# Kernel tuning notes

Hardware: AMD Instinct MI355X
Metric: run time of the kernel (lower is better)

The kernel has to match this reference:

```python
import jax, jax.numpy as jnp
import numpy as np

BLOCK_M, BLOCK_K = 16, 64
THRES = 0.8


def setup_inputs() -> dict:
    key = jax.random.key(0)
    kx, kw = jax.random.split(key)
    bsz, seq, in_f, out_f = 128, 1, 4096, 11008
    x = jax.random.normal(kx, (bsz, seq, in_f), dtype=jnp.float16)
    # kaiming_uniform_(a=sqrt(5)) on a (in,out) weight -> bound = 1/sqrt(fan_in)
    bound = 1.0 / np.sqrt(in_f)
    weight = jax.random.uniform(kw, (in_f, out_f), dtype=jnp.float16,
                                minval=-bound, maxval=bound)
    bias = jnp.zeros((out_f,), dtype=jnp.float16)
    return {"x": x, "weight": weight, "bias": bias}


def reference(x, weight, bias):
    bsz, seq, hidden = x.shape
    x2 = x.reshape(bsz * seq, hidden)          # (M, K), seq == 1 decode path
    M, K = x2.shape
    # avg_magnitude_threshold: per (BLOCK_M, BLOCK_K) block mean |x| vs thres
    blocks = x2.reshape(M // BLOCK_M, BLOCK_M, K // BLOCK_K, BLOCK_K)
    avg = jnp.mean(jnp.abs(blocks).astype(jnp.float32), axis=(1, 3))  # (M/bm, K/bk)
    mask = avg > THRES                           # block active if avg magnitude above thres
    # blocksparse_masked_gemm: skipped blocks contribute nothing -> zero them out
    xm = jnp.where(mask[:, None, :, None], blocks, jnp.float16(0)).reshape(M, K)
    y = xm @ weight                              # (M, out_features)
    return y.reshape(bsz, seq, -1) + bias
```

## Files before the change

### kernel.cpp

```cpp
#include <hip/hip_runtime.h>
#include <stdint.h>

using f32x4   = __attribute__((ext_vector_type(4))) float;
using short8  = __attribute__((ext_vector_type(8))) short;
using float4v = __attribute__((ext_vector_type(4))) float;
using float2v = __attribute__((ext_vector_type(2))) float;
using uint2v  = __attribute__((ext_vector_type(2))) unsigned int;

#define NCOL 11008
#define KDIM 4096
#define LSTRIDE 264

__device__ __forceinline__ unsigned pk_bf16(float a, float b) {
  unsigned ua = __float_as_uint(a); ua += 0x7fffu + ((ua >> 16) & 1u);
  unsigned ub = __float_as_uint(b); ub += 0x7fffu + ((ub >> 16) & 1u);
  return (ua >> 16) | (ub & 0xffff0000u);
}

__global__ __launch_bounds__(256) void mask_kernel(const float* __restrict__ x,
                                                   unsigned* __restrict__ mask16) {
  const int rb  = blockIdx.x >> 2;
  const int grp = blockIdx.x & 3;
  const int t   = threadIdx.x;
  __shared__ double part[256];
  double s = 0.0;
#pragma unroll 4
  for (int i = 0; i < 16; ++i) {
    const float* p = x + (size_t)(rb * 16 + i) * KDIM + grp * 1024 + t * 4;
    float4v a = *(const float4v*)p;
    s += (double)fabsf(a[0]) + (double)fabsf(a[1]) +
         (double)fabsf(a[2]) + (double)fabsf(a[3]);
  }
  part[t] = s;
  __syncthreads();
  if (t < 16) {
    double acc = 0.0;
#pragma unroll
    for (int u = 0; u < 16; ++u) acc += part[t * 16 + u];
    bool on = (acc * (1.0 / 1024.0)) > (double)0.8f;
    unsigned long long bal = __ballot(on);
    if (t == 0) mask16[blockIdx.x] = (unsigned)(bal & 0xffffu);
  }
}

__global__ __launch_bounds__(256) void gemm_kernel(
    const float* __restrict__ x, const float* __restrict__ w,
    const float* __restrict__ bias, const unsigned* __restrict__ mask16,
    float* __restrict__ out) {

  __shared__ __align__(16) uint8_t lds[64 * LSTRIDE];

  const int tid  = threadIdx.x;
  const int lane = tid & 63;
  const int wv   = tid >> 6;
  const int c    = lane & 15;
  const int q    = lane >> 4;
  const int rb   = blockIdx.x;
  const int n0   = blockIdx.y * 128;

  unsigned long long bm = 0;
#pragma unroll
  for (int g = 0; g < 4; ++g)
    bm |= ((unsigned long long)mask16[rb * 4 + g]) << (16 * g);

  f32x4 acc[2] = {};

  const int sk = tid >> 5;
  const int sn = (tid & 31) * 4;
  uint8_t* wS = lds + (size_t)sk * LSTRIDE + sn * 2;

  for (int kb = 0; kb < 64; ++kb) {
    if (!((bm >> kb) & 1ull)) continue;

    const float* wp = w + (size_t)(kb * 64 + sk) * NCOL + n0 + sn;
    float4v wr[8];
#pragma unroll
    for (int r = 0; r < 8; ++r)
      wr[r] = *(const float4v*)(wp + (size_t)r * 8 * NCOL);

    __syncthreads();
#pragma unroll
    for (int r = 0; r < 8; ++r) {
      uint2v v;
      v[0] = pk_bf16(wr[r][0], wr[r][1]);
      v[1] = pk_bf16(wr[r][2], wr[r][3]);
      *(uint2v*)(wS + (size_t)r * 8 * LSTRIDE) = v;
    }
    __syncthreads();

#pragma unroll
    for (int ks = 0; ks < 2; ++ks) {
      const float* xp = x + (size_t)(rb * 16 + c) * KDIM + kb * 64 + ks * 32 + q * 8;
      float4v xa = *(const float4v*)xp;
      float4v xb = *(const float4v*)(xp + 4);
      union { short8 v; unsigned u[4]; } af;
      af.u[0] = pk_bf16(xa[0], xa[1]);
      af.u[1] = pk_bf16(xa[2], xa[3]);
      af.u[2] = pk_bf16(xb[0], xb[1]);
      af.u[3] = pk_bf16(xb[2], xb[3]);

      const uint8_t* wb = lds + (size_t)(ks * 32 + q * 8) * LSTRIDE + (wv * 32 + 2 * c) * 2;
      unsigned wj[8];
#pragma unroll
      for (int j = 0; j < 8; ++j)
        wj[j] = *(const unsigned*)(wb + (size_t)j * LSTRIDE);
      union { short8 v; unsigned u[4]; } be, bo;
#pragma unroll
      for (int p = 0; p < 4; ++p) {
        be.u[p] = (wj[2 * p] & 0x0000ffffu) | (wj[2 * p + 1] << 16);
        bo.u[p] = (wj[2 * p] >> 16) | (wj[2 * p + 1] & 0xffff0000u);
      }
      acc[0] = __builtin_amdgcn_mfma_f32_16x16x32_bf16(af.v, be.v, acc[0], 0, 0, 0);
      acc[1] = __builtin_amdgcn_mfma_f32_16x16x32_bf16(af.v, bo.v, acc[1], 0, 0, 0);
    }
  }

  const int colE = n0 + wv * 32 + 2 * c;
  const float bE = bias[colE];
  const float bO = bias[colE + 1];
#pragma unroll
  for (int p = 0; p < 4; ++p) {
    const int row = rb * 16 + q * 4 + p;
    float2v st;
    st[0] = acc[0][p] + bE;
    st[1] = acc[1][p] + bO;
    *(float2v*)(out + (size_t)row * NCOL + colE) = st;
  }
}

extern "C" void kernel_launch(void* const* d_in, const int* in_sizes, int n_in,
                              void* d_out, int out_size, void* d_ws, size_t ws_size,
                              hipStream_t stream) {
  const float* x    = (const float*)d_in[0];
  const float* w    = (const float*)d_in[1];
  const float* bias = (const float*)d_in[2];
  float* out        = (float*)d_out;
  unsigned* mask16  = (unsigned*)d_ws;

  hipLaunchKernelGGL(mask_kernel, dim3(32), dim3(256), 0, stream, x, mask16);
  hipLaunchKernelGGL(gemm_kernel, dim3(8, 86), dim3(256), 0, stream,
                     x, w, bias, mask16, out);
}
```

Measured before the change: 298.7 us.

## Prefetch next active block's weights and activations while computing current block

The GEMM loop now walks only the set bits of the block mask using ctz, and issues the global loads for the next active K-block right after the current block's weights are written to LDS, so those loads overlap the MFMA work. Activation loads are also hoisted into registers as part of this prefetch. The mask kernel's row loop is fully unrolled. The cost is higher register pressure from holding the prefetched weight and activation registers alongside the current block's data.

```diff
diff --git a/kernel.cpp b/kernel.cpp
--- a/kernel.cpp
+++ b/kernel.cpp
@@ -24,7 +24,7 @@
   const int t   = threadIdx.x;
   __shared__ double part[256];
   double s = 0.0;
-#pragma unroll 4
+#pragma unroll
   for (int i = 0; i < 16; ++i) {
     const float* p = x + (size_t)(rb * 16 + i) * KDIM + grp * 1024 + t * 4;
     float4v a = *(const float4v*)p;
@@ -68,15 +68,31 @@
   const int sk = tid >> 5;
   const int sn = (tid & 31) * 4;
   uint8_t* wS = lds + (size_t)sk * LSTRIDE + sn * 2;
+  const float* xrow = x + (size_t)(rb * 16 + c) * KDIM + q * 8;
 
-  for (int kb = 0; kb < 64; ++kb) {
-    if (!((bm >> kb) & 1ull)) continue;
+  float4v wr[8];
+  float4v xr[4];
 
-    const float* wp = w + (size_t)(kb * 64 + sk) * NCOL + n0 + sn;
-    float4v wr[8];
-#pragma unroll
-    for (int r = 0; r < 8; ++r)
-      wr[r] = *(const float4v*)(wp + (size_t)r * 8 * NCOL);
+#define ISSUE(KB)                                                        \
+  {                                                                      \
+    const float* wp = w + (size_t)((KB)*64 + sk) * NCOL + n0 + sn;       \
+    _Pragma("unroll")                                                    \
+    for (int r = 0; r < 8; ++r)                                          \
+      wr[r] = *(const float4v*)(wp + (size_t)r * 8 * NCOL);              \
+    const float* xp = xrow + (KB)*64;                                    \
+    xr[0] = *(const float4v*)(xp);                                       \
+    xr[1] = *(const float4v*)(xp + 4);                                   \
+    xr[2] = *(const float4v*)(xp + 32);                                  \
+    xr[3] = *(const float4v*)(xp + 36);                                  \
+  }
+
+  unsigned long long rem = bm;
+  int kb = -1;
+  if (rem) { kb = __builtin_ctzll(rem); rem &= rem - 1; ISSUE(kb); }
+
+  while (kb >= 0) {
+    int kbn = -1;
+    if (rem) { kbn = __builtin_ctzll(rem); rem &= rem - 1; }
 
     __syncthreads();
 #pragma unroll
@@ -88,16 +104,23 @@
     }
     __syncthreads();
 
+    float4v xs0 = xr[0], xs1 = xr[1], xs2 = xr[2], xs3 = xr[3];
+    if (kbn >= 0) ISSUE(kbn);
+
 #pragma unroll
     for (int ks = 0; ks < 2; ++ks) {
-      const float* xp = x + (size_t)(rb * 16 + c) * KDIM + kb * 64 + ks * 32 + q * 8;
-      float4v xa = *(const float4v*)xp;
-      float4v xb = *(const float4v*)(xp + 4);
       union { short8 v; unsigned u[4]; } af;
-      af.u[0] = pk_bf16(xa[0], xa[1]);
-      af.u[1] = pk_bf16(xa[2], xa[3]);
-      af.u[2] = pk_bf16(xb[0], xb[1]);
-      af.u[3] = pk_bf16(xb[2], xb[3]);
+      if (ks == 0) {
+        af.u[0] = pk_bf16(xs0[0], xs0[1]);
+        af.u[1] = pk_bf16(xs0[2], xs0[3]);
+        af.u[2] = pk_bf16(xs1[0], xs1[1]);
+        af.u[3] = pk_bf16(xs1[2], xs1[3]);
+      } else {
+        af.u[0] = pk_bf16(xs2[0], xs2[1]);
+        af.u[1] = pk_bf16(xs2[2], xs2[3]);
+        af.u[2] = pk_bf16(xs3[0], xs3[1]);
+        af.u[3] = pk_bf16(xs3[2], xs3[3]);
+      }
 
       const uint8_t* wb = lds + (size_t)(ks * 32 + q * 8) * LSTRIDE + (wv * 32 + 2 * c) * 2;
       unsigned wj[8];
@@ -113,7 +136,9 @@
       acc[0] = __builtin_amdgcn_mfma_f32_16x16x32_bf16(af.v, be.v, acc[0], 0, 0, 0);
       acc[1] = __builtin_amdgcn_mfma_f32_16x16x32_bf16(af.v, bo.v, acc[1], 0, 0, 0);
     }
+    kb = kbn;
   }
+#undef ISSUE
 
   const int colE = n0 + wv * 32 + 2 * c;
   const float bE = bias[colE];
```

Measured after the change: 303.1 us. About the same (+1.5%).

## Pre-convert masked activations to bf16 and split-K GEMM with full-M weight reuse

Applied to the files above, without the earlier changes.

A combined kernel now computes the block mask and writes zeroed-or-converted bf16 activations to the workspace. The GEMM no longer skips inactive K blocks per row block. Each workgroup covers all 128 rows for a 128-column tile and a 512-wide K slice, so each weight tile is loaded once instead of eight times, with a software prefetch of the next weight tile. Partial sums go to the output through float atomics after a memset, which adds a memset launch and atomic traffic and gives up per-row-block sparsity skipping.

```diff
diff --git a/kernel.cpp b/kernel.cpp
--- a/kernel.cpp
+++ b/kernel.cpp
@@ -6,6 +6,7 @@
 using float4v = __attribute__((ext_vector_type(4))) float;
 using float2v = __attribute__((ext_vector_type(2))) float;
 using uint2v  = __attribute__((ext_vector_type(2))) unsigned int;
+using uint4v  = __attribute__((ext_vector_type(4))) unsigned int;
 
 #define NCOL 11008
 #define KDIM 4096
@@ -17,36 +18,45 @@
   return (ua >> 16) | (ub & 0xffff0000u);
 }
 
-__global__ __launch_bounds__(256) void mask_kernel(const float* __restrict__ x,
-                                                   unsigned* __restrict__ mask16) {
-  const int rb  = blockIdx.x >> 2;
-  const int grp = blockIdx.x & 3;
-  const int t   = threadIdx.x;
+__global__ __launch_bounds__(256) void mask_convert_kernel(
+    const float* __restrict__ x, unsigned* __restrict__ xbf) {
+  const int rb = blockIdx.x;
+  const int g  = blockIdx.y;
+  const int t  = threadIdx.x;
   __shared__ double part[256];
+  __shared__ unsigned sh_bits;
+
+  const float* base = x + (size_t)rb * 16 * KDIM + g * 512 + t * 2;
   double s = 0.0;
-#pragma unroll 4
-  for (int i = 0; i < 16; ++i) {
-    const float* p = x + (size_t)(rb * 16 + i) * KDIM + grp * 1024 + t * 4;
-    float4v a = *(const float4v*)p;
-    s += (double)fabsf(a[0]) + (double)fabsf(a[1]) +
-         (double)fabsf(a[2]) + (double)fabsf(a[3]);
+#pragma unroll
+  for (int r = 0; r < 16; ++r) {
+    float2v a = *(const float2v*)(base + (size_t)r * KDIM);
+    s += (double)fabsf(a[0]) + (double)fabsf(a[1]);
   }
   part[t] = s;
   __syncthreads();
-  if (t < 16) {
+  if (t < 8) {
     double acc = 0.0;
 #pragma unroll
-    for (int u = 0; u < 16; ++u) acc += part[t * 16 + u];
+    for (int u = 0; u < 32; ++u) acc += part[t * 32 + u];
     bool on = (acc * (1.0 / 1024.0)) > (double)0.8f;
     unsigned long long bal = __ballot(on);
-    if (t == 0) mask16[blockIdx.x] = (unsigned)(bal & 0xffffu);
+    if (t == 0) sh_bits = (unsigned)(bal & 0xffu);
+  }
+  __syncthreads();
+  const unsigned keep = (sh_bits >> (t >> 5)) & 1u;
+
+  unsigned* dst = xbf + (size_t)rb * 16 * (KDIM / 2) + g * 256 + t;
+#pragma unroll
+  for (int r = 0; r < 16; ++r) {
+    float2v a = *(const float2v*)(base + (size_t)r * KDIM);
+    dst[(size_t)r * (KDIM / 2)] = keep ? pk_bf16(a[0], a[1]) : 0u;
   }
 }
 
 __global__ __launch_bounds__(256) void gemm_kernel(
-    const float* __restrict__ x, const float* __restrict__ w,
-    const float* __restrict__ bias, const unsigned* __restrict__ mask16,
-    float* __restrict__ out) {
+    const unsigned* __restrict__ xbf, const float* __restrict__ w,
+    const float* __restrict__ bias, float* __restrict__ out) {
 
   __shared__ __align__(16) uint8_t lds[64 * LSTRIDE];
 
@@ -55,29 +65,28 @@
   const int wv   = tid >> 6;
   const int c    = lane & 15;
   const int q    = lane >> 4;
-  const int rb   = blockIdx.x;
-  const int n0   = blockIdx.y * 128;
+  const int n0   = blockIdx.x * 128;
+  const int kz   = blockIdx.y;
 
-  unsigned long long bm = 0;
-#pragma unroll
-  for (int g = 0; g < 4; ++g)
-    bm |= ((unsigned long long)mask16[rb * 4 + g]) << (16 * g);
-
-  f32x4 acc[2] = {};
+  f32x4 acc[8][2] = {};
 
   const int sk = tid >> 5;
   const int sn = (tid & 31) * 4;
   uint8_t* wS = lds + (size_t)sk * LSTRIDE + sn * 2;
 
-  for (int kb = 0; kb < 64; ++kb) {
-    if (!((bm >> kb) & 1ull)) continue;
+  float4v wr[8];
+#define ISSUE_W(KB)                                                      \
+  {                                                                      \
+    const float* wp = w + (size_t)(kz * 512 + (KB)*64 + sk) * NCOL + n0 + sn; \
+    _Pragma("unroll")                                                    \
+    for (int r = 0; r < 8; ++r)                                          \
+      wr[r] = *(const float4v*)(wp + (size_t)r * 8 * NCOL);              \
+  }
 
-    const float* wp = w + (size_t)(kb * 64 + sk) * NCOL + n0 + sn;
-    float4v wr[8];
-#pragma unroll
-    for (int r = 0; r < 8; ++r)
-      wr[r] = *(const float4v*)(wp + (size_t)r * 8 * NCOL);
+  const uint4v* aBase = (const uint4v*)xbf + (size_t)c * 512 + kz * 64 + q;
 
+  ISSUE_W(0);
+  for (int kb = 0; kb < 8; ++kb) {
     __syncthreads();
 #pragma unroll
     for (int r = 0; r < 8; ++r) {
@@ -87,17 +96,14 @@
       *(uint2v*)(wS + (size_t)r * 8 * LSTRIDE) = v;
     }
     __syncthreads();
+    if (kb < 7) ISSUE_W(kb + 1);
 
 #pragma unroll
     for (int ks = 0; ks < 2; ++ks) {
-      const float* xp = x + (size_t)(rb * 16 + c) * KDIM + kb * 64 + ks * 32 + q * 8;
-      float4v xa = *(const float4v*)xp;
-      float4v xb = *(const float4v*)(xp + 4);
-      union { short8 v; unsigned u[4]; } af;
-      af.u[0] = pk_bf16(xa[0], xa[1]);
-      af.u[1] = pk_bf16(xa[2], xa[3]);
-      af.u[2] = pk_bf16(xb[0], xb[1]);
-      af.u[3] = pk_bf16(xb[2], xb[3]);
+      union { uint4v u; short8 v; } am[8];
+#pragma unroll
+      for (int mt = 0; mt < 8; ++mt)
+        am[mt].u = aBase[(size_t)mt * 16 * 512 + kb * 8 + ks * 4];
 
       const uint8_t* wb = lds + (size_t)(ks * 32 + q * 8) * LSTRIDE + (wv * 32 + 2 * c) * 2;
       unsigned wj[8];
@@ -110,21 +116,27 @@
         be.u[p] = (wj[2 * p] & 0x0000ffffu) | (wj[2 * p + 1] << 16);
         bo.u[p] = (wj[2 * p] >> 16) | (wj[2 * p + 1] & 0xffff0000u);
       }
-      acc[0] = __builtin_amdgcn_mfma_f32_16x16x32_bf16(af.v, be.v, acc[0], 0, 0, 0);
-      acc[1] = __builtin_amdgcn_mfma_f32_16x16x32_bf16(af.v, bo.v, acc[1], 0, 0, 0);
+#pragma unroll
+      for (int mt = 0; mt < 8; ++mt) {
+        acc[mt][0] = __builtin_amdgcn_mfma_f32_16x16x32_bf16(am[mt].v, be.v, acc[mt][0], 0, 0, 0);
+        acc[mt][1] = __builtin_amdgcn_mfma_f32_16x16x32_bf16(am[mt].v, bo.v, acc[mt][1], 0, 0, 0);
+      }
     }
   }
+#undef ISSUE_W
 
   const int colE = n0 + wv * 32 + 2 * c;
-  const float bE = bias[colE];
-  const float bO = bias[colE + 1];
+  const float bE = (kz == 0) ? bias[colE] : 0.f;
+  const float bO = (kz == 0) ? bias[colE + 1] : 0.f;
 #pragma unroll
-  for (int p = 0; p < 4; ++p) {
-    const int row = rb * 16 + q * 4 + p;
-    float2v st;
-    st[0] = acc[0][p] + bE;
-    st[1] = acc[1][p] + bO;
-    *(float2v*)(out + (size_t)row * NCOL + colE) = st;
+  for (int mt = 0; mt < 8; ++mt) {
+#pragma unroll
+    for (int p = 0; p < 4; ++p) {
+      const int row = mt * 16 + q * 4 + p;
+      float* o = out + (size_t)row * NCOL + colE;
+      unsafeAtomicAdd(o,     acc[mt][0][p] + bE);
+      unsafeAtomicAdd(o + 1, acc[mt][1][p] + bO);
+    }
   }
 }
 
@@ -135,9 +147,10 @@
   const float* w    = (const float*)d_in[1];
   const float* bias = (const float*)d_in[2];
   float* out        = (float*)d_out;
-  unsigned* mask16  = (unsigned*)d_ws;
+  unsigned* xbf     = (unsigned*)d_ws;
 
-  hipLaunchKernelGGL(mask_kernel, dim3(32), dim3(256), 0, stream, x, mask16);
-  hipLaunchKernelGGL(gemm_kernel, dim3(8, 86), dim3(256), 0, stream,
-                     x, w, bias, mask16, out);
+  hipLaunchKernelGGL(mask_convert_kernel, dim3(8, 8), dim3(256), 0, stream, x, xbf);
+  hipMemsetAsync(out, 0, (size_t)out_size * sizeof(float), stream);
+  hipLaunchKernelGGL(gemm_kernel, dim3(86, 8), dim3(256), 0, stream,
+                     xbf, w, bias, out);
 }
```

New measurement: 329.9 us. 1.1x slower.
